# Performance work log

Hardware: AMD Instinct MI355X
Metric: run time of the kernel (lower is better)

The kernel has to match this reference:

```python
import jax, jax.numpy as jnp
import numpy as np


def _topk_masked_softmax(attn, k):
    # Keep only the top-k entries per row (last dim), softmax over them.
    _, idx = jax.lax.top_k(attn, k)  # [b, nh, C, k]
    mask = jnp.put_along_axis(
        jnp.zeros(attn.shape, dtype=bool), idx, True, axis=-1, inplace=False
    )
    return jax.nn.softmax(jnp.where(mask, attn, -jnp.inf), axis=-1)


def setup_inputs() -> dict:
    key = jax.random.key(0)
    k0, k1, k2, k3, k4 = jax.random.split(key, 5)
    b, nh, C = 8, 8, 512
    attn = jax.random.normal(k0, (b, nh, C, C), dtype=jnp.float32)
    # In the torch module these are Parameters initialized to 0.2; use random
    # positive scalars of similar scale for a non-degenerate baseline.
    w1 = jax.random.uniform(k1, (1,), dtype=jnp.float32)
    w2 = jax.random.uniform(k2, (1,), dtype=jnp.float32)
    w3 = jax.random.uniform(k3, (1,), dtype=jnp.float32)
    w4 = jax.random.uniform(k4, (1,), dtype=jnp.float32)
    return {"attn": attn, "w1": w1, "w2": w2, "w3": w3, "w4": w4}


def reference(attn, w1, w2, w3, w4):
    C = attn.shape[-1]
    a1 = _topk_masked_softmax(attn, int(C / 2))
    a2 = _topk_masked_softmax(attn, int(C * 2 / 3))
    a3 = _topk_masked_softmax(attn, int(C * 3 / 4))
    a4 = _topk_masked_softmax(attn, int(C * 4 / 5))
    return a1 * w1 + a2 * w2 + a3 * w3 + a4 * w4
```

## Files before the change

### kernel.cpp

```cpp
#include <hip/hip_runtime.h>
#include <math.h>

#define ROW_C 512
#define NBIN 2048
#define NPACK (NBIN / 2)

__global__ __launch_bounds__(256) void topk_ms_kernel(
    const float* __restrict__ attn,
    const float* __restrict__ w1p, const float* __restrict__ w2p,
    const float* __restrict__ w3p, const float* __restrict__ w4p,
    float* __restrict__ out)
{
    __shared__ __align__(16) unsigned hist_all[4][NPACK];

    const int lane = threadIdx.x & 63;
    const int wv   = threadIdx.x >> 6;
    unsigned* h = hist_all[wv];
    int4* hv = (int4*)h;

    const long long row  = (long long)blockIdx.x * 4 + wv;
    const long long base = row * ROW_C + lane * 8;

    const float4 A = *reinterpret_cast<const float4*>(attn + base);
    const float4 B = *reinterpret_cast<const float4*>(attn + base + 4);
    float orig[8] = {A.x, A.y, A.z, A.w, B.x, B.y, B.z, B.w};

    unsigned key[8];
    int bin[8];
    #pragma unroll
    for (int s = 0; s < 8; ++s) {
        const unsigned u = __float_as_uint(orig[s]);
        key[s] = (u & 0x80000000u) ? ~u : (u | 0x80000000u);
        const float y = fminf(fmaxf(orig[s], -7.9f), 7.9f) + 24.0f;
        bin[s] = (int)((__float_as_uint(y) >> 12) & 0x7FFu);
    }

    {
        const int4 z = make_int4(0, 0, 0, 0);
        hv[lane] = z; hv[lane + 64] = z; hv[lane + 128] = z; hv[lane + 192] = z;
    }

    #pragma unroll
    for (int s = 0; s < 8; ++s) {
        const int j  = bin[s] >> 1;
        const int ph = j ^ (((j >> 5) & 7) << 2);
        atomicAdd(&h[ph], (bin[s] & 1) ? 0x10000u : 1u);
    }

    unsigned pp[16];
    #pragma unroll
    for (int k = 0; k < 4; ++k) {
        const int b  = 4 * lane + k;
        const int pb = b ^ ((b >> 3) & 7);
        const int4 v = hv[pb];
        pp[4 * k]     = (unsigned)v.x;
        pp[4 * k + 1] = (unsigned)v.y;
        pp[4 * k + 2] = (unsigned)v.z;
        pp[4 * k + 3] = (unsigned)v.w;
    }
    unsigned run = 0;
    #pragma unroll
    for (int j = 0; j < 16; ++j) {
        const unsigned q = pp[j] + (pp[j] << 16);
        pp[j] = q + run * 0x10001u;
        run = pp[j] >> 16;
    }
    unsigned incl = run;
    #pragma unroll
    for (int off = 1; off < 64; off <<= 1) {
        const unsigned t = __shfl_up(incl, off, 64);
        if (lane >= off) incl += t;
    }
    const unsigned bmul = (incl - run) * 0x10001u;
    #pragma unroll
    for (int j = 0; j < 16; ++j) pp[j] += bmul;
    #pragma unroll
    for (int k = 0; k < 4; ++k) {
        const int b  = 4 * lane + k;
        const int pb = b ^ ((b >> 3) & 7);
        hv[pb] = make_int4((int)pp[4 * k], (int)pp[4 * k + 1],
                           (int)pp[4 * k + 2], (int)pp[4 * k + 3]);
    }

    int bsel = 0, Rwithin = 0;
    if (lane < 4) {
        const int KS[4] = {256, 341, 384, 409};
        const int K = KS[lane];
        const int T = 512 - K + 1;
        int lo = -1, hi = NBIN - 1;
        unsigned pbv = 512u;
        #pragma unroll
        for (int it = 0; it < 11; ++it) {
            const int mid = (lo + hi) >> 1;
            const int jm  = mid >> 1;
            const int ph  = jm ^ (((jm >> 5) & 7) << 2);
            const unsigned w  = h[ph];
            const unsigned pv = (mid & 1) ? (w >> 16) : (w & 0xFFFFu);
            const bool ge = ((int)pv >= T);
            hi  = ge ? mid : hi;
            pbv = ge ? pv  : pbv;
            lo  = ge ? lo  : mid;
        }
        bsel    = hi;
        Rwithin = K - 512 + (int)pbv;
    }

    int b_r[4], R_r[4];
    #pragma unroll
    for (int r = 0; r < 4; ++r) {
        b_r[r] = __shfl(bsel, r, 64);
        R_r[r] = __shfl(Rwithin, r, 64);
    }

    unsigned tk[4]; int need[4], cnteq[4];
    #pragma unroll
    for (int r = 0; r < 4; ++r) {
        unsigned cm[8];
        #pragma unroll
        for (int s = 0; s < 8; ++s)
            cm[s] = (bin[s] == b_r[r]) ? key[s] : 0u;
        int R = R_r[r];
        unsigned t; int c;
        while (true) {
            unsigned mk = cm[0];
            #pragma unroll
            for (int s = 1; s < 8; ++s) mk = (cm[s] > mk) ? cm[s] : mk;
            #pragma unroll
            for (int off = 32; off >= 1; off >>= 1) {
                const unsigned o = __shfl_xor(mk, off, 64);
                mk = (o > mk) ? o : mk;
            }
            t = mk;
            c = 0;
            #pragma unroll
            for (int s = 0; s < 8; ++s)
                c += (int)__popcll(__ballot(cm[s] == t));
            if (c >= R) break;
            R -= c;
            #pragma unroll
            for (int s = 0; s < 8; ++s)
                if (cm[s] == t) cm[s] = 0u;
        }
        tk[r] = t; need[r] = R; cnteq[r] = c;
    }

    int fl[8] = {0, 0, 0, 0, 0, 0, 0, 0};
    #pragma unroll
    for (int r = 0; r < 4; ++r) {
        const unsigned t = tk[r];
        if (need[r] == cnteq[r]) {
            #pragma unroll
            for (int s = 0; s < 8; ++s)
                fl[s] |= ((int)(key[s] >= t)) << r;
        } else {
            const unsigned long long ltm = (1ull << lane) - 1ull;
            int basec = 0;
            #pragma unroll
            for (int s = 0; s < 8; ++s)
                basec += (int)__popcll(__ballot(key[s] == t) & ltm);
            int own = 0;
            #pragma unroll
            for (int s = 0; s < 8; ++s) {
                const bool eq = (key[s] == t);
                if (key[s] > t || (eq && (basec + own) < need[r]))
                    fl[s] |= (1 << r);
                own += eq ? 1 : 0;
            }
        }
    }

    float eo[8];
    #pragma unroll
    for (int s = 0; s < 8; ++s) eo[s] = __expf(orig[s]);

    float z0 = 0.f, z1 = 0.f, z2 = 0.f, z3 = 0.f;
    #pragma unroll
    for (int s = 0; s < 8; ++s) {
        z0 += (fl[s] & 1) ? eo[s] : 0.f;
        z1 += (fl[s] & 2) ? eo[s] : 0.f;
        z2 += (fl[s] & 4) ? eo[s] : 0.f;
        z3 += (fl[s] & 8) ? eo[s] : 0.f;
    }
    #pragma unroll
    for (int off = 32; off >= 1; off >>= 1) {
        z0 += __shfl_xor(z0, off, 64);
        z1 += __shfl_xor(z1, off, 64);
        z2 += __shfl_xor(z2, off, 64);
        z3 += __shfl_xor(z3, off, 64);
    }

    const float wz0 = w1p[0] / z0;
    const float wz1 = w2p[0] / z1;
    const float wz2 = w3p[0] / z2;
    const float wz3 = w4p[0] / z3;

    float res[8];
    #pragma unroll
    for (int s = 0; s < 8; ++s) {
        float c = 0.f;
        c += (fl[s] & 1) ? wz0 : 0.f;
        c += (fl[s] & 2) ? wz1 : 0.f;
        c += (fl[s] & 4) ? wz2 : 0.f;
        c += (fl[s] & 8) ? wz3 : 0.f;
        res[s] = eo[s] * c;
    }
    *reinterpret_cast<float4*>(out + base)     = make_float4(res[0], res[1], res[2], res[3]);
    *reinterpret_cast<float4*>(out + base + 4) = make_float4(res[4], res[5], res[6], res[7]);
}

extern "C" void kernel_launch(void* const* d_in, const int* in_sizes, int n_in,
                              void* d_out, int out_size, void* d_ws, size_t ws_size,
                              hipStream_t stream) {
    const float* attn = (const float*)d_in[0];
    const float* w1   = (const float*)d_in[1];
    const float* w2   = (const float*)d_in[2];
    const float* w3   = (const float*)d_in[3];
    const float* w4   = (const float*)d_in[4];
    float* out = (float*)d_out;

    int rows = in_sizes[0] / ROW_C;
    int blocks = (rows + 3) / 4;
    topk_ms_kernel<<<blocks, 256, 0, stream>>>(attn, w1, w2, w3, w4, out);
}
```

Before: 148.1 us.

## Use ballot-based bin search and interleave four top-k threshold refinements

The serial 11-step binary search over the prefix histogram, which ran on four lanes, is replaced by wave-wide ballots over the per-lane inclusive prefix and a second ballot within the owner's 16 packed words. The four per-k iterative max-extraction loops are merged into one loop so their shuffle reductions interleave, using a running cutoff instead of clearing candidates. The flag computation gains a tie-free fast path, and the divisions become hardware reciprocal approximations. The aim is to shorten the serial latency per wave, at the cost of slightly less precise normalisation from rcp.

Measured after the change: 166.4 us. 12.3% more time.

```diff
diff --git a/kernel.cpp b/kernel.cpp
--- a/kernel.cpp
+++ b/kernel.cpp
@@ -82,89 +82,110 @@
                            (int)pp[4 * k + 2], (int)pp[4 * k + 3]);
     }
 
-    int bsel = 0, Rwithin = 0;
-    if (lane < 4) {
-        const int KS[4] = {256, 341, 384, 409};
-        const int K = KS[lane];
-        const int T = 512 - K + 1;
-        int lo = -1, hi = NBIN - 1;
-        unsigned pbv = 512u;
-        #pragma unroll
-        for (int it = 0; it < 11; ++it) {
-            const int mid = (lo + hi) >> 1;
-            const int jm  = mid >> 1;
-            const int ph  = jm ^ (((jm >> 5) & 7) << 2);
-            const unsigned w  = h[ph];
-            const unsigned pv = (mid & 1) ? (w >> 16) : (w & 0xFFFFu);
-            const bool ge = ((int)pv >= T);
-            hi  = ge ? mid : hi;
-            pbv = ge ? pv  : pbv;
-            lo  = ge ? lo  : mid;
-        }
-        bsel    = hi;
-        Rwithin = K - 512 + (int)pbv;
-    }
-
+    const int KS[4] = {256, 341, 384, 409};
     int b_r[4], R_r[4];
+    const int w15 = lane & 15;
     #pragma unroll
     for (int r = 0; r < 4; ++r) {
-        b_r[r] = __shfl(bsel, r, 64);
-        R_r[r] = __shfl(Rwithin, r, 64);
-    }
-
-    unsigned tk[4]; int need[4], cnteq[4];
-    #pragma unroll
-    for (int r = 0; r < 4; ++r) {
-        unsigned cm[8];
-        #pragma unroll
-        for (int s = 0; s < 8; ++s)
-            cm[s] = (bin[s] == b_r[r]) ? key[s] : 0u;
-        int R = R_r[r];
-        unsigned t; int c;
-        while (true) {
-            unsigned mk = cm[0];
+        const int T = 513 - KS[r];
+        const unsigned long long ob = __ballot((int)incl >= T);
+        const int owner = __ffsll(ob) - 1;
+        const int g  = (owner << 4) | w15;
+        const int pg = g ^ (((g >> 5) & 7) << 2);
+        const unsigned pv = h[pg];
+        const int lo = (int)(pv & 0xFFFFu), hi = (int)(pv >> 16);
+        const unsigned bl = (unsigned)__ballot(lo >= T) & 0xFFFFu;
+        const unsigned bh = (unsigned)__ballot(hi >= T) & 0xFFFFu;
+        const int binl_l = bl ? (2 * (__ffs(bl) - 1)) : 1000;
+        const int binl_h = 2 * (__ffs(bh) - 1) + 1;
+        const int binl = min(binl_l, binl_h);
+        const unsigned pvs = __shfl(pv, binl >> 1, 64);
+        const int pref = (binl & 1) ? (int)(pvs >> 16) : (int)(pvs & 0xFFFFu);
+        b_r[r] = (owner << 5) + binl;
+        R_r[r] = KS[r] - 512 + pref;
+    }
+
+    unsigned tk[4];
+    int need[4], cnteq[4];
+    unsigned tcut[4] = {0xFFFFFFFFu, 0xFFFFFFFFu, 0xFFFFFFFFu, 0xFFFFFFFFu};
+    int done = 0;
+    while (done != 15) {
+        unsigned lmax[4];
+        #pragma unroll
+        for (int r = 0; r < 4; ++r) {
+            unsigned mk = 0;
             #pragma unroll
-            for (int s = 1; s < 8; ++s) mk = (cm[s] > mk) ? cm[s] : mk;
+            for (int s = 0; s < 8; ++s) {
+                const unsigned v =
+                    (bin[s] == b_r[r] && key[s] < tcut[r]) ? key[s] : 0u;
+                mk = (v > mk) ? v : mk;
+            }
+            lmax[r] = mk;
+        }
+        #pragma unroll
+        for (int off = 32; off >= 1; off >>= 1) {
             #pragma unroll
-            for (int off = 32; off >= 1; off >>= 1) {
-                const unsigned o = __shfl_xor(mk, off, 64);
-                mk = (o > mk) ? o : mk;
-            }
-            t = mk;
-            c = 0;
+            for (int r = 0; r < 4; ++r) {
+                const unsigned o = __shfl_xor(lmax[r], off, 64);
+                lmax[r] = (o > lmax[r]) ? o : lmax[r];
+            }
+        }
+        int cnt[4];
+        #pragma unroll
+        for (int r = 0; r < 4; ++r) {
+            int c = 0;
             #pragma unroll
             for (int s = 0; s < 8; ++s)
-                c += (int)__popcll(__ballot(cm[s] == t));
-            if (c >= R) break;
-            R -= c;
-            #pragma unroll
-            for (int s = 0; s < 8; ++s)
-                if (cm[s] == t) cm[s] = 0u;
-        }
-        tk[r] = t; need[r] = R; cnteq[r] = c;
+                c += (int)__popcll(__ballot(key[s] == lmax[r]));
+            cnt[r] = c;
+        }
+        #pragma unroll
+        for (int r = 0; r < 4; ++r) {
+            if (!(done & (1 << r))) {
+                if (cnt[r] >= R_r[r]) {
+                    tk[r] = lmax[r]; need[r] = R_r[r]; cnteq[r] = cnt[r];
+                    done |= (1 << r);
+                } else {
+                    R_r[r] -= cnt[r];
+                    tcut[r] = lmax[r];
+                }
+            }
+        }
     }
 
     int fl[8] = {0, 0, 0, 0, 0, 0, 0, 0};
-    #pragma unroll
-    for (int r = 0; r < 4; ++r) {
-        const unsigned t = tk[r];
-        if (need[r] == cnteq[r]) {
-            #pragma unroll
-            for (int s = 0; s < 8; ++s)
-                fl[s] |= ((int)(key[s] >= t)) << r;
-        } else {
-            const unsigned long long ltm = (1ull << lane) - 1ull;
-            int basec = 0;
-            #pragma unroll
-            for (int s = 0; s < 8; ++s)
-                basec += (int)__popcll(__ballot(key[s] == t) & ltm);
-            int own = 0;
-            #pragma unroll
-            for (int s = 0; s < 8; ++s) {
-                const bool eq = (key[s] == t);
-                if (key[s] > t || (eq && (basec + own) < need[r]))
-                    fl[s] |= (1 << r);
-                own += eq ? 1 : 0;
+    const bool anytie = (need[0] != cnteq[0]) | (need[1] != cnteq[1]) |
+                        (need[2] != cnteq[2]) | (need[3] != cnteq[3]);
+    if (!anytie) {
+        #pragma unroll
+        for (int s = 0; s < 8; ++s) {
+            fl[s] = (int)(key[s] >= tk[0])
+                  | ((int)(key[s] >= tk[1]) << 1)
+                  | ((int)(key[s] >= tk[2]) << 2)
+                  | ((int)(key[s] >= tk[3]) << 3);
+        }
+    } else {
+        const unsigned long long ltm = (1ull << lane) - 1ull;
+        #pragma unroll
+        for (int r = 0; r < 4; ++r) {
+            const unsigned t = tk[r];
+            if (need[r] == cnteq[r]) {
+                #pragma unroll
+                for (int s = 0; s < 8; ++s)
+                    fl[s] |= ((int)(key[s] >= t)) << r;
+            } else {
+                int basec = 0;
+                #pragma unroll
+                for (int s = 0; s < 8; ++s)
+                    basec += (int)__popcll(__ballot(key[s] == t) & ltm);
+                int own = 0;
+                #pragma unroll
+                for (int s = 0; s < 8; ++s) {
+                    const bool eq = (key[s] == t);
+                    if (key[s] > t || (eq && (basec + own) < need[r]))
+                        fl[s] |= (1 << r);
+                    own += eq ? 1 : 0;
+                }
             }
         }
     }
@@ -189,10 +210,10 @@
         z3 += __shfl_xor(z3, off, 64);
     }
 
-    const float wz0 = w1p[0] / z0;
-    const float wz1 = w2p[0] / z1;
-    const float wz2 = w3p[0] / z2;
-    const float wz3 = w4p[0] / z3;
+    const float wz0 = w1p[0] * __builtin_amdgcn_rcpf(z0);
+    const float wz1 = w2p[0] * __builtin_amdgcn_rcpf(z1);
+    const float wz2 = w3p[0] * __builtin_amdgcn_rcpf(z2);
+    const float wz3 = w4p[0] * __builtin_amdgcn_rcpf(z3);
 
     float res[8];
     #pragma unroll
```
